# Kernel tuning notes

Measured on AMD Instinct MI355X. Metric: run time of the kernel, lower is better.

Reference implementation:

```python
import jax, jax.numpy as jnp
import numpy as np

VOCAB = 50257
B, V, HID, OUT = 32, 1024, 768, 256


def setup_inputs() -> dict:
    key = jax.random.key(0)
    k1, k2, k3, k4, k5 = jax.random.split(key, 5)
    emb_table = jax.random.normal(k1, (VOCAB, HID), dtype=jnp.float32) * 0.02
    adj = jax.random.uniform(k2, (B, V, V), dtype=jnp.float32)
    fc_w = jax.random.normal(k3, (OUT, HID), dtype=jnp.float32) * (1.0 / np.sqrt(HID))
    fc_b = jax.random.normal(k4, (OUT,), dtype=jnp.float32) * 0.01
    gv_ids = jax.random.randint(k5, (B, V), 0, VOCAB, dtype=jnp.int64)
    return {"emb_table": emb_table, "adj": adj, "fc_w": fc_w, "fc_b": fc_b, "gv_ids": gv_ids}


def reference(emb_table, adj, fc_w, fc_b, gv_ids):
    # Per-sample embedding gather: [B, V, HID]
    gvocab_ev = emb_table[gv_ids]
    # adj @ E, then mean over node rows -> fuse: sum over both node axes / V
    # H_vh = adj[b] @ E[b]  (V,V)@(V,HID); graph_embed = H_vh.mean(axis=0)
    h = jnp.einsum('bvw,bwh->bh', adj, gvocab_ev) / V  # [B, HID]
    # fc_hg linear (activation=None, dropout disabled)
    out = h @ fc_w.T + fc_b  # [B, OUT]
    return out
```

## Files before the change

### kernel.cpp

```cpp
#include <hip/hip_runtime.h>

#define B   32
#define V   1024
#define HID 768
#define OUT 256
#define NVC 16


__global__ void colsum_partial_kernel(const float* __restrict__ adj,
                                      float* __restrict__ partial,
                                      float* __restrict__ h) {
    const int b   = blockIdx.x;
    const int vc  = blockIdx.y;
    const int tid = threadIdx.x;
    const float4* adj4 = reinterpret_cast<const float4*>(adj)
                       + (size_t)(b * V + vc * 64) * (V / 4);
    float4 acc = make_float4(0.f, 0.f, 0.f, 0.f);
    #pragma unroll 4
    for (int v = 0; v < 64; ++v) {
        float4 a = adj4[(size_t)v * (V / 4) + tid];
        acc.x += a.x; acc.y += a.y; acc.z += a.z; acc.w += a.w;
    }
    reinterpret_cast<float4*>(partial + (size_t)(b * NVC + vc) * V)[tid] = acc;
    if (vc < 3)
        h[b * HID + vc * 256 + tid] = 0.f;
}

__global__ void gather_wsum_kernel(const float* __restrict__ emb,
                                   const int* __restrict__ ids,
                                   const float* __restrict__ partial,
                                   float* __restrict__ h) {
    const int b  = blockIdx.x;
    const int wc = blockIdx.y;
    const int t  = threadIdx.x;
    __shared__ float sm[4][32];
    __shared__ float c_s[32];
    __shared__ int   ids_s[32];
    if (t < 128) {
        const int wi = t & 31, q = t >> 5;
        float s = 0.f;
        #pragma unroll
        for (int j = 0; j < 4; ++j)
            s += partial[(size_t)(b * NVC + q * 4 + j) * V + wc * 32 + wi];
        sm[q][wi] = s;
    }
    if (t < 32)
        ids_s[t] = ids[b * V + wc * 32 + t];
    __syncthreads();
    if (t < 32)
        c_s[t] = sm[0][t] + sm[1][t] + sm[2][t] + sm[3][t];
    __syncthreads();
    float4 acc = make_float4(0.f, 0.f, 0.f, 0.f);
    #pragma unroll 4
    for (int i = 0; i < 32; ++i) {
        const float4* T4 = reinterpret_cast<const float4*>(emb + (size_t)ids_s[i] * HID);
        const float4 a = T4[t];
        const float  s = c_s[i];
        acc.x += s * a.x; acc.y += s * a.y; acc.z += s * a.z; acc.w += s * a.w;
    }
    float* hb = h + b * HID + t * 4;
    atomicAdd(hb + 0, acc.x);
    atomicAdd(hb + 1, acc.y);
    atomicAdd(hb + 2, acc.z);
    atomicAdd(hb + 3, acc.w);
}


__global__ void colsum_atomic_kernel(const float* __restrict__ adj, float* __restrict__ c) {
    const int b   = blockIdx.x;
    const int vc  = blockIdx.y;
    const int tid = threadIdx.x;
    const float4* adj4 = reinterpret_cast<const float4*>(adj) + (size_t)b * V * (V / 4);
    float4 acc = make_float4(0.f, 0.f, 0.f, 0.f);
    const int v0 = vc * 64;
    #pragma unroll 4
    for (int v = v0; v < v0 + 64; ++v) {
        float4 a = adj4[(size_t)v * (V / 4) + tid];
        acc.x += a.x; acc.y += a.y; acc.z += a.z; acc.w += a.w;
    }
    float* cb = c + b * V + tid * 4;
    atomicAdd(cb + 0, acc.x);
    atomicAdd(cb + 1, acc.y);
    atomicAdd(cb + 2, acc.z);
    atomicAdd(cb + 3, acc.w);
}

__global__ void gather_wsum_direct_kernel(const float* __restrict__ emb,
                                          const int* __restrict__ ids,
                                          const float* __restrict__ c,
                                          float* __restrict__ h) {
    const int b  = blockIdx.x;
    const int wc = blockIdx.y;
    const int t  = threadIdx.x;
    __shared__ float c_s[32];
    __shared__ int   ids_s[32];
    if (t < 32) {
        ids_s[t] = ids[b * V + wc * 32 + t];
        c_s[t]   = c[b * V + wc * 32 + t];
    }
    __syncthreads();
    float4 acc = make_float4(0.f, 0.f, 0.f, 0.f);
    #pragma unroll 4
    for (int i = 0; i < 32; ++i) {
        const float4* T4 = reinterpret_cast<const float4*>(emb + (size_t)ids_s[i] * HID);
        const float4 a = T4[t];
        const float  s = c_s[i];
        acc.x += s * a.x; acc.y += s * a.y; acc.z += s * a.z; acc.w += s * a.w;
    }
    float* hb = h + b * HID + t * 4;
    atomicAdd(hb + 0, acc.x);
    atomicAdd(hb + 1, acc.y);
    atomicAdd(hb + 2, acc.z);
    atomicAdd(hb + 3, acc.w);
}


__global__ void fc_kernel(const float* __restrict__ h,
                          const float* __restrict__ fc_w,
                          const float* __restrict__ fc_b,
                          float* __restrict__ out) {
    const int b    = blockIdx.x;
    const int wave = threadIdx.x >> 6;
    const int lane = threadIdx.x & 63;
    const int o    = blockIdx.y * 4 + wave;
    __shared__ float h_s[HID];
    for (int i = threadIdx.x; i < HID; i += 256) h_s[i] = h[b * HID + i];
    __syncthreads();
    const float* wrow = fc_w + (size_t)o * HID;
    float acc = 0.f;
    #pragma unroll
    for (int k = 0; k < HID / 64; ++k)
        acc += wrow[k * 64 + lane] * h_s[k * 64 + lane];
    #pragma unroll
    for (int off = 32; off > 0; off >>= 1)
        acc += __shfl_down(acc, off, 64);
    if (lane == 0)
        out[b * OUT + o] = fc_b[o] + acc * (1.0f / V);
}

extern "C" void kernel_launch(void* const* d_in, const int* in_sizes, int n_in,
                              void* d_out, int out_size, void* d_ws, size_t ws_size,
                              hipStream_t stream) {
    const float* emb  = (const float*)d_in[0];
    const float* adj  = (const float*)d_in[1];
    const float* fc_w = (const float*)d_in[2];
    const float* fc_b = (const float*)d_in[3];
    const int*   ids  = (const int*)d_in[4];
    float* out = (float*)d_out;

    const size_t needA = (size_t)(B * NVC * V + B * HID) * sizeof(float);

    if (ws_size >= needA) {
        float* partial = (float*)d_ws;
        float* h       = partial + B * NVC * V;
        colsum_partial_kernel<<<dim3(B, NVC), 256, 0, stream>>>(adj, partial, h);
        gather_wsum_kernel<<<dim3(B, 32), 192, 0, stream>>>(emb, ids, partial, h);
        fc_kernel<<<dim3(B, OUT / 4), 256, 0, stream>>>(h, fc_w, fc_b, out);
    } else {
        float* c = (float*)d_ws;
        float* h = c + B * V;
        hipMemsetAsync(d_ws, 0, (size_t)(B * V + B * HID) * sizeof(float), stream);
        colsum_atomic_kernel<<<dim3(B, NVC), 256, 0, stream>>>(adj, c);
        gather_wsum_direct_kernel<<<dim3(B, 32), 192, 0, stream>>>(emb, ids, c, h);
        fc_kernel<<<dim3(B, OUT / 4), 256, 0, stream>>>(h, fc_w, fc_b, out);
    }
}
```

Baseline: 54.02 us.

## Replace atomic accumulation of h with partial buffers reduced in FC kernel

The gather kernel now writes per-chunk partial sums of h to a workspace buffer instead of issuing float atomicAdds. A new FC kernel reduces the 32 partials into shared memory and then computes 32 outputs per block, which cuts the grid from B x 64 to B x 8 blocks. The zero-init of h is dropped from the colsum kernel and two unroll factors are raised. In exchange, each FC block re-reads 96KB of partials, and the workspace requirement grows.

```diff
diff --git a/kernel.cpp b/kernel.cpp
--- a/kernel.cpp
+++ b/kernel.cpp
@@ -5,31 +5,29 @@
 #define HID 768
 #define OUT 256
 #define NVC 16
+#define NWC 32
 
 
 __global__ void colsum_partial_kernel(const float* __restrict__ adj,
-                                      float* __restrict__ partial,
-                                      float* __restrict__ h) {
+                                      float* __restrict__ partial) {
     const int b   = blockIdx.x;
     const int vc  = blockIdx.y;
     const int tid = threadIdx.x;
     const float4* adj4 = reinterpret_cast<const float4*>(adj)
                        + (size_t)(b * V + vc * 64) * (V / 4);
     float4 acc = make_float4(0.f, 0.f, 0.f, 0.f);
-    #pragma unroll 4
+    #pragma unroll 8
     for (int v = 0; v < 64; ++v) {
         float4 a = adj4[(size_t)v * (V / 4) + tid];
         acc.x += a.x; acc.y += a.y; acc.z += a.z; acc.w += a.w;
     }
     reinterpret_cast<float4*>(partial + (size_t)(b * NVC + vc) * V)[tid] = acc;
-    if (vc < 3)
-        h[b * HID + vc * 256 + tid] = 0.f;
 }
 
 __global__ void gather_wsum_kernel(const float* __restrict__ emb,
                                    const int* __restrict__ ids,
                                    const float* __restrict__ partial,
-                                   float* __restrict__ h) {
+                                   float* __restrict__ hpart) {
     const int b  = blockIdx.x;
     const int wc = blockIdx.y;
     const int t  = threadIdx.x;
@@ -51,18 +49,51 @@
         c_s[t] = sm[0][t] + sm[1][t] + sm[2][t] + sm[3][t];
     __syncthreads();
     float4 acc = make_float4(0.f, 0.f, 0.f, 0.f);
-    #pragma unroll 4
+    #pragma unroll 8
     for (int i = 0; i < 32; ++i) {
         const float4* T4 = reinterpret_cast<const float4*>(emb + (size_t)ids_s[i] * HID);
         const float4 a = T4[t];
         const float  s = c_s[i];
         acc.x += s * a.x; acc.y += s * a.y; acc.z += s * a.z; acc.w += s * a.w;
     }
-    float* hb = h + b * HID + t * 4;
-    atomicAdd(hb + 0, acc.x);
-    atomicAdd(hb + 1, acc.y);
-    atomicAdd(hb + 2, acc.z);
-    atomicAdd(hb + 3, acc.w);
+    reinterpret_cast<float4*>(hpart + (size_t)(b * NWC + wc) * HID)[t] = acc;
+}
+
+__global__ void fc_reduce_kernel(const float* __restrict__ hpart,
+                                 const float* __restrict__ fc_w,
+                                 const float* __restrict__ fc_b,
+                                 float* __restrict__ out) {
+    const int b  = blockIdx.x;
+    const int og = blockIdx.y;
+    const int t  = threadIdx.x;
+    __shared__ float h_s[HID];
+    {
+        const float* hp = hpart + (size_t)b * NWC * HID;
+        float s0 = 0.f, s1 = 0.f, s2 = 0.f;
+        #pragma unroll 8
+        for (int j = 0; j < NWC; ++j) {
+            s0 += hp[j * HID + t];
+            s1 += hp[j * HID + t + 256];
+            s2 += hp[j * HID + t + 512];
+        }
+        h_s[t] = s0; h_s[t + 256] = s1; h_s[t + 512] = s2;
+    }
+    __syncthreads();
+    const int wave = t >> 6, lane = t & 63;
+    #pragma unroll
+    for (int it = 0; it < 8; ++it) {
+        const int o = og * 32 + it * 4 + wave;
+        const float* wrow = fc_w + (size_t)o * HID;
+        float acc = 0.f;
+        #pragma unroll
+        for (int k = 0; k < HID / 64; ++k)
+            acc += wrow[k * 64 + lane] * h_s[k * 64 + lane];
+        #pragma unroll
+        for (int off = 32; off > 0; off >>= 1)
+            acc += __shfl_down(acc, off, 64);
+        if (lane == 0)
+            out[b * OUT + o] = fc_b[o] + acc * (1.0f / V);
+    }
 }
 
 
@@ -114,11 +145,10 @@
     atomicAdd(hb + 3, acc.w);
 }
 
-
-__global__ void fc_kernel(const float* __restrict__ h,
-                          const float* __restrict__ fc_w,
-                          const float* __restrict__ fc_b,
-                          float* __restrict__ out) {
+__global__ void fc_direct_kernel(const float* __restrict__ h,
+                                 const float* __restrict__ fc_w,
+                                 const float* __restrict__ fc_b,
+                                 float* __restrict__ out) {
     const int b    = blockIdx.x;
     const int wave = threadIdx.x >> 6;
     const int lane = threadIdx.x & 63;
@@ -148,20 +178,20 @@
     const int*   ids  = (const int*)d_in[4];
     float* out = (float*)d_out;
 
-    const size_t needA = (size_t)(B * NVC * V + B * HID) * sizeof(float);
+    const size_t needA = (size_t)(B * NVC * V + B * NWC * HID) * sizeof(float);
 
     if (ws_size >= needA) {
         float* partial = (float*)d_ws;
-        float* h       = partial + B * NVC * V;
-        colsum_partial_kernel<<<dim3(B, NVC), 256, 0, stream>>>(adj, partial, h);
-        gather_wsum_kernel<<<dim3(B, 32), 192, 0, stream>>>(emb, ids, partial, h);
-        fc_kernel<<<dim3(B, OUT / 4), 256, 0, stream>>>(h, fc_w, fc_b, out);
+        float* hpart   = partial + B * NVC * V;
+        colsum_partial_kernel<<<dim3(B, NVC), 256, 0, stream>>>(adj, partial);
+        gather_wsum_kernel<<<dim3(B, NWC), 192, 0, stream>>>(emb, ids, partial, hpart);
+        fc_reduce_kernel<<<dim3(B, 8), 256, 0, stream>>>(hpart, fc_w, fc_b, out);
     } else {
         float* c = (float*)d_ws;
         float* h = c + B * V;
         hipMemsetAsync(d_ws, 0, (size_t)(B * V + B * HID) * sizeof(float), stream);
         colsum_atomic_kernel<<<dim3(B, NVC), 256, 0, stream>>>(adj, c);
-        gather_wsum_direct_kernel<<<dim3(B, 32), 192, 0, stream>>>(emb, ids, c, h);
-        fc_kernel<<<dim3(B, OUT / 4), 256, 0, stream>>>(h, fc_w, fc_b, out);
+        gather_wsum_direct_kernel<<<dim3(B, NWC), 192, 0, stream>>>(emb, ids, c, h);
+        fc_direct_kernel<<<dim3(B, OUT / 4), 256, 0, stream>>>(h, fc_w, fc_b, out);
     }
 }
```

Result: faster. 49.42 us (-8.5%).
